# Kernel tuning notes

Measured on AMD Instinct MI355X. Metric: run time of the kernel, lower is better.

Reference implementation:

```python
import jax, jax.numpy as jnp
import numpy as np

BH, S, D = 32, 2048, 128

def setup_inputs() -> dict:
    key = jax.random.key(0)
    k1, k2, k3, k4 = jax.random.split(key, 4)
    q = jax.random.normal(k1, (BH, S, D), dtype=jnp.float32)
    k = jax.random.normal(k2, (BH, S, D), dtype=jnp.float32)
    v = jax.random.normal(k3, (BH, S, D), dtype=jnp.float32)
    scale_factor = jax.random.normal(k4, (S, S), dtype=jnp.float32)
    return {"q": q, "k": k, "v": v, "scale_factor": scale_factor, "dropout_p": 1}

def reference(q, k, v, scale_factor, dropout_p):
    # qk: [BH, Sq, Sk]
    qk = jnp.einsum('bqd,bkd->bqk', q, k)
    scaled_qk = qk * scale_factor  # per-element (non-scalar) scale, broadcast over BH
    p = jax.nn.softmax(scaled_qk, axis=-1)
    # Dropout(p=0.0) is identity; then mul by scalar dropout_p
    p = p * dropout_p
    out = jnp.einsum('bqk,bkd->bqd', p, v)
    return out
```

## Files before the change

### kernel.cpp

```cpp
#include <hip/hip_runtime.h>

#define S_LEN 2048
#define D_DIM 128
#define BQ 128
#define BK 32
#define NITER (S_LEN / BK)
#define NITER2 (NITER / 2)

typedef float f32x4 __attribute__((ext_vector_type(4)));
typedef short s16x8 __attribute__((ext_vector_type(8)));
typedef short s16x4 __attribute__((ext_vector_type(4)));
typedef unsigned int u32;

#if __has_builtin(__builtin_amdgcn_exp2f)
#define EXP2(x) __builtin_amdgcn_exp2f(x)
#else
#define EXP2(x) exp2f(x)
#endif

__device__ __forceinline__ u32 pack_trunc(float x0, float x1) {
    return __builtin_amdgcn_perm(__float_as_uint(x1), __float_as_uint(x0), 0x07060302u);
}
__device__ __forceinline__ u32 pack_rne(float x0, float x1) {
    return __builtin_amdgcn_perm(__float_as_uint(x1) + 0x8000u,
                                 __float_as_uint(x0) + 0x8000u, 0x07060302u);
}

#define GLOAD16(g, l) \
    __builtin_amdgcn_global_load_lds((const __attribute__((address_space(1))) u32*)(g), \
                                     (__attribute__((address_space(3))) u32*)(l), 16, 0, 0)

#if __has_builtin(__builtin_amdgcn_mfma_f32_16x16x16bf16_1k)
__device__ __forceinline__ f32x4 MFMA16(s16x4 a, s16x4 b, f32x4 c) {
    return __builtin_amdgcn_mfma_f32_16x16x16bf16_1k(a, b, c, 0, 0, 0);
}
#else
__device__ __forceinline__ f32x4 MFMA16(s16x4 a, s16x4 b, f32x4 c) {
    asm("v_mfma_f32_16x16x16_bf16 %0, %1, %2, %0" : "+v"(c) : "v"(a), "v"(b));
    return c;
}
#endif

#if __has_builtin(__builtin_amdgcn_permlane16_swap) && __has_builtin(__builtin_amdgcn_permlane32_swap)
#define BFLY(x, OP)                                                                       \
    {                                                                                     \
        auto p_ = __builtin_amdgcn_permlane16_swap(__float_as_uint(x), __float_as_uint(x), false, false); \
        x = OP(__uint_as_float(p_[0]), __uint_as_float(p_[1]));                           \
        auto q_ = __builtin_amdgcn_permlane32_swap(__float_as_uint(x), __float_as_uint(x), false, false); \
        x = OP(__uint_as_float(q_[0]), __uint_as_float(q_[1]));                           \
    }
#else
#define BFLY(x, OP)                      \
    {                                    \
        x = OP(x, __shfl_xor(x, 16));    \
        x = OP(x, __shfl_xor(x, 32));    \
    }
#endif
__device__ __forceinline__ float fadd_(float a, float b) { return a + b; }

__global__ void prep_k(const float* __restrict__ K, unsigned short* __restrict__ Kc) {
    const int t  = blockIdx.x * 256 + threadIdx.x;
    const int c  = t & 15;
    const int s  = (t >> 4) & (S_LEN - 1);
    const int bh = t >> 15;
    const float* src = K + ((size_t)bh * S_LEN + s) * D_DIM + c * 8;
    const float4 a = *(const float4*)src;
    const float4 b = *(const float4*)(src + 4);
    const float x[8] = {a.x,a.y,a.z,a.w,b.x,b.y,b.z,b.w};
    u32 h[4], l[4];
    #pragma unroll
    for (int i = 0; i < 4; ++i) {
        const float x0 = x[2*i], x1 = x[2*i+1];
        h[i] = pack_trunc(x0, x1);
        const float r0 = x0 - __uint_as_float(__float_as_uint(x0) & 0xFFFF0000u);
        const float r1 = x1 - __uint_as_float(__float_as_uint(x1) & 0xFFFF0000u);
        l[i] = pack_trunc(r0, r1);
    }
    const int kt = s >> 5, r = s & 31, rl = r & 7;
    unsigned short* base = Kc + ((((size_t)bh * NITER + kt) * 32 + r) << 8);
    *(uint4*)(base + (((2*c)     ^ rl) << 3)) = make_uint4(h[0],h[1],h[2],h[3]);
    *(uint4*)(base + (((2*c + 1) ^ rl) << 3)) = make_uint4(l[0],l[1],l[2],l[3]);
}

__global__ void prep_v(const float* __restrict__ V, unsigned short* __restrict__ Vt) {
    const int t  = blockIdx.x * 256 + threadIdx.x;
    const int d  = t & 127;
    const int kt = (t >> 7) & (NITER - 1);
    const int bh = t >> 13;
    const float* src = V + (((size_t)bh * NITER + kt) * BK) * D_DIM + d;
    const int dt = d >> 4, lr = d & 15;
    unsigned short* base = Vt + ((((size_t)bh * NITER + kt) * 8 + dt) << 9);
    #pragma unroll
    for (int q = 0; q < 4; ++q) {
        u32 w0 = pack_rne(src[(q*4+0) * D_DIM],    src[(q*4+1) * D_DIM]);
        u32 w1 = pack_rne(src[(q*4+2) * D_DIM],    src[(q*4+3) * D_DIM]);
        u32 w2 = pack_rne(src[(16+q*4+0) * D_DIM], src[(16+q*4+1) * D_DIM]);
        u32 w3 = pack_rne(src[(16+q*4+2) * D_DIM], src[(16+q*4+3) * D_DIM]);
        *(uint4*)(base + ((q * 16 + lr) << 3)) = make_uint4(w0, w1, w2, w3);
    }
}

__global__ __launch_bounds__(512, 2)
void attn_fused(const float* __restrict__ Q, const unsigned short* __restrict__ Kc,
                const unsigned short* __restrict__ Vt, const float* __restrict__ SF,
                const int* __restrict__ DP, float* __restrict__ OUT)
{
    __shared__ __align__(16) unsigned short sK[2][2][32 * 256];
    __shared__ float mlx[4][2][16][2];

    const int bh   = blockIdx.y;
    const int q0   = blockIdx.x * BQ;
    const int tid  = threadIdx.x;
    const int w    = tid >> 6;
    const int par  = w >> 2;
    const int wq   = w & 3;
    const int lane = tid & 63;
    const int quad = lane >> 4;
    const int lr   = lane & 15;
    const int rl   = lr & 7;

    const size_t bh_off = (size_t)bh * S_LEN * D_DIM;
    const float LOG2E = 1.4426950408889634f;

    s16x8 qhi[2][4], qlo[2][4];
    int qrow[2];
    #pragma unroll
    for (int g = 0; g < 2; ++g) {
        qrow[g] = q0 + wq * 32 + g * 16 + lr;
        const float* qr = Q + bh_off + (size_t)qrow[g] * D_DIM + quad * 8;
        #pragma unroll
        for (int d0 = 0; d0 < 4; ++d0) {
            const float4 u0 = *(const float4*)(qr + d0 * 32);
            const float4 u1 = *(const float4*)(qr + d0 * 32 + 4);
            const float x[8] = {u0.x,u0.y,u0.z,u0.w,u1.x,u1.y,u1.z,u1.w};
            union { u32 w4[4]; s16x8 v; } H, L;
            #pragma unroll
            for (int i = 0; i < 4; ++i) {
                const float x0 = x[2*i], x1 = x[2*i+1];
                H.w4[i] = pack_trunc(x0, x1);
                const float r0 = x0 - __uint_as_float(__float_as_uint(x0) & 0xFFFF0000u);
                const float r1 = x1 - __uint_as_float(__float_as_uint(x1) & 0xFFFF0000u);
                L.w4[i] = pack_trunc(r0, r1);
            }
            qhi[g][d0] = H.v; qlo[g][d0] = L.v;
        }
    }

    f32x4 Oacc[2][8] = {};
    float mrow[2] = {-INFINITY, -INFINITY};
    float lrow[2] = {0.f, 0.f};

    const unsigned short* KtBase = Kc + (((size_t)bh * NITER) << 13);
    const unsigned short* VtBase = Vt + (((size_t)bh * NITER) << 12) + (lane << 3);

    {
        const unsigned short* K0 = KtBase + ((size_t)par << 13);
        #pragma unroll
        for (int i = 0; i < 4; ++i)
            GLOAD16(K0 + (wq * 4 + i) * 512 + lane * 8, &sK[0][par][(wq * 4 + i) * 512]);
    }

    const float* sfq[2];
    f32x4 sf0[2], sf1[2];
    {
        const f32x4 l2e = {LOG2E, LOG2E, LOG2E, LOG2E};
        #pragma unroll
        for (int g = 0; g < 2; ++g) {
            sfq[g] = SF + (size_t)qrow[g] * S_LEN + quad * 4;
            sf0[g] = *(const f32x4*)(sfq[g] + par * 32) * l2e;
            sf1[g] = *(const f32x4*)(sfq[g] + par * 32 + 16) * l2e;
        }
    }

    for (int it = 0; it < NITER2; ++it) {
        const int p = it & 1;
        __syncthreads();

        uint4 vreg[8];
        {
            const unsigned short* Vk = VtBase + ((size_t)(2 * it + par) << 12);
            #pragma unroll
            for (int dt = 0; dt < 8; ++dt)
                vreg[dt] = *(const uint4*)(Vk + (dt << 9));
        }

        f32x4 nf0[2], nf1[2];
        const bool more = (it + 1 < NITER2);
        if (more) {
            const unsigned short* Kn = KtBase + ((size_t)(2 * it + 2 + par) << 13);
            #pragma unroll
            for (int i = 0; i < 4; ++i)
                GLOAD16(Kn + (wq * 4 + i) * 512 + lane * 8, &sK[1 - p][par][(wq * 4 + i) * 512]);
            const f32x4 l2e = {LOG2E, LOG2E, LOG2E, LOG2E};
            #pragma unroll
            for (int g = 0; g < 2; ++g) {
                nf0[g] = *(const f32x4*)(sfq[g] + (2 * it + 2 + par) * 32) * l2e;
                nf1[g] = *(const f32x4*)(sfq[g] + (2 * it + 2 + par) * 32 + 16) * l2e;
            }
        }

        const unsigned short* sKp = sK[p][par];
        f32x4 acc[2][2] = {};
        __builtin_amdgcn_s_setprio(1);
        #pragma unroll
        for (int nt = 0; nt < 2; ++nt) {
            const unsigned short* rowp = sKp + (nt * 16 + lr) * 256;
            #pragma unroll
            for (int d0 = 0; d0 < 4; ++d0) {
                const int uh = (8 * d0 + 2 * quad) ^ rl;
                const s16x8 kh8 = *(const s16x8*)(rowp + (uh << 3));
                const s16x8 kl8 = *(const s16x8*)(rowp + ((uh ^ 1) << 3));
                #pragma unroll
                for (int g = 0; g < 2; ++g) {
                    acc[g][nt] = __builtin_amdgcn_mfma_f32_16x16x32_bf16(kh8, qlo[g][d0], acc[g][nt], 0, 0, 0);
                    acc[g][nt] = __builtin_amdgcn_mfma_f32_16x16x32_bf16(kl8, qhi[g][d0], acc[g][nt], 0, 0, 0);
                    acc[g][nt] = __builtin_amdgcn_mfma_f32_16x16x32_bf16(kh8, qhi[g][d0], acc[g][nt], 0, 0, 0);
                }
            }
        }
        __builtin_amdgcn_s_setprio(0);

        union PB { u32 w2[2]; s16x4 v; } B0[2], B1[2];
        #pragma unroll
        for (int g = 0; g < 2; ++g) {
            const f32x4 t0 = acc[g][0] * sf0[g];
            const f32x4 t1 = acc[g][1] * sf1[g];
            float mx = fmaxf(fmaxf(fmaxf(t0[0], t0[1]), fmaxf(t0[2], t0[3])),
                             fmaxf(fmaxf(t1[0], t1[1]), fmaxf(t1[2], t1[3])));
            BFLY(mx, fmaxf);
            const float mnew = fmaxf(mrow[g], mx);
            if (!__all(mnew == mrow[g])) {
                const float al = EXP2(mrow[g] - mnew);
                mrow[g] = mnew;
                lrow[g] *= al;
                const f32x4 alv = {al, al, al, al};
                #pragma unroll
                for (int dt = 0; dt < 8; ++dt)
                    Oacc[g][dt] *= alv;
            }
            const float m = mrow[g];
            f32x4 P0, P1;
            #pragma unroll
            for (int r = 0; r < 4; ++r) {
                P0[r] = EXP2(t0[r] - m);
                P1[r] = EXP2(t1[r] - m);
            }
            float rs = ((P0[0] + P0[1]) + (P0[2] + P0[3])) + ((P1[0] + P1[1]) + (P1[2] + P1[3]));
            BFLY(rs, fadd_);
            lrow[g] += rs;
            B0[g].w2[0] = pack_rne(P0[0], P0[1]); B0[g].w2[1] = pack_rne(P0[2], P0[3]);
            B1[g].w2[0] = pack_rne(P1[0], P1[1]); B1[g].w2[1] = pack_rne(P1[2], P1[3]);
        }

        __builtin_amdgcn_s_setprio(1);
        #pragma unroll
        for (int dt = 0; dt < 8; ++dt) {
            union { uint4 u; struct { s16x4 a0; s16x4 a1; } s; } vv;
            vv.u = vreg[dt];
            #pragma unroll
            for (int g = 0; g < 2; ++g) {
                Oacc[g][dt] = MFMA16(vv.s.a0, B0[g].v, Oacc[g][dt]);
                Oacc[g][dt] = MFMA16(vv.s.a1, B1[g].v, Oacc[g][dt]);
            }
        }
        __builtin_amdgcn_s_setprio(0);

        if (more) {
            #pragma unroll
            for (int g = 0; g < 2; ++g) { sf0[g] = nf0[g]; sf1[g] = nf1[g]; }
        }
    }

    __syncthreads();
    float* obuf = (float*)&sK[0][0][0];
    if (par) {
        #pragma unroll
        for (int g = 0; g < 2; ++g) {
            mlx[wq][g][lr][0] = mrow[g];
            mlx[wq][g][lr][1] = lrow[g];
            #pragma unroll
            for (int dt = 0; dt < 8; ++dt)
                *(f32x4*)(obuf + ((((wq * 2 + g) * 8 + dt) * 64 + lane) << 2)) = Oacc[g][dt];
        }
    }
    __syncthreads();
    if (!par) {
        const float dpf = (float)DP[0];
        #pragma unroll
        for (int g = 0; g < 2; ++g) {
            const float m_o = mlx[wq][g][lr][0];
            const float l_o = mlx[wq][g][lr][1];
            const float ms  = fmaxf(mrow[g], m_o);
            const float se  = EXP2(mrow[g] - ms);
            const float so  = EXP2(m_o - ms);
            const float ls  = se * lrow[g] + so * l_o;
            const float fe  = se * dpf / ls;
            const float fo  = so * dpf / ls;
            const f32x4 fev = {fe, fe, fe, fe};
            const f32x4 fov = {fo, fo, fo, fo};
            float* orow = OUT + bh_off + (size_t)qrow[g] * D_DIM + quad * 4;
            #pragma unroll
            for (int dt = 0; dt < 8; ++dt) {
                const f32x4 oo = *(const f32x4*)(obuf + ((((wq * 2 + g) * 8 + dt) * 64 + lane) << 2));
                const f32x4 o = Oacc[g][dt] * fev + oo * fov;
                *(f32x4*)(orow + dt * 16) = o;
            }
        }
    }
}

extern "C" void kernel_launch(void* const* d_in, const int* in_sizes, int n_in,
                              void* d_out, int out_size, void* d_ws, size_t ws_size,
                              hipStream_t stream) {
    const float* q  = (const float*)d_in[0];
    const float* k  = (const float*)d_in[1];
    const float* v  = (const float*)d_in[2];
    const float* sf = (const float*)d_in[3];
    const int*   dp = (const int*)d_in[4];
    float* out = (float*)d_out;

    const size_t kc_ushorts = (size_t)32 * NITER * 32 * 256;
    unsigned short* Kc = (unsigned short*)d_ws;
    unsigned short* Vt = Kc + kc_ushorts;

    prep_k<<<4096, 256, 0, stream>>>(k, Kc);
    prep_v<<<1024, 256, 0, stream>>>(v, Vt);
    dim3 grid(S_LEN / BQ, 32);
    attn_fused<<<grid, dim3(512), 0, stream>>>(q, Kc, Vt, sf, dp, out);
}
```

Before: 382.8 us.

## Halve query tile and split KV tiles into 16-key halves per wave pair

The query block shrinks from 128 to 64 rows with 256-thread blocks instead of 512. The two wave groups now split each 32-key K/V tile into two 16-key halves rather than taking alternate whole tiles. This halves shared memory and per-wave accumulator and V-register use, which should allow more resident blocks and smaller, more numerous blocks for load balance. The cost is more blocks and smaller MFMA work per sync, and each loop iteration now does half the work, so barrier and softmax overhead per key rises.

```diff
diff --git a/kernel.cpp b/kernel.cpp
--- a/kernel.cpp
+++ b/kernel.cpp
@@ -2,10 +2,10 @@
 
 #define S_LEN 2048
 #define D_DIM 128
-#define BQ 128
+#define BQ 64
 #define BK 32
 #define NITER (S_LEN / BK)
-#define NITER2 (NITER / 2)
+#define HITER 64
 
 typedef float f32x4 __attribute__((ext_vector_type(4)));
 typedef short s16x8 __attribute__((ext_vector_type(8)));
@@ -100,20 +100,20 @@
     }
 }
 
-__global__ __launch_bounds__(512, 2)
+__global__ __launch_bounds__(256, 4)
 void attn_fused(const float* __restrict__ Q, const unsigned short* __restrict__ Kc,
                 const unsigned short* __restrict__ Vt, const float* __restrict__ SF,
                 const int* __restrict__ DP, float* __restrict__ OUT)
 {
-    __shared__ __align__(16) unsigned short sK[2][2][32 * 256];
-    __shared__ float mlx[4][2][16][2];
+    __shared__ __align__(16) unsigned short sK[2][2][16 * 256];
+    __shared__ float mlx[2][2][16][2];
 
     const int bh   = blockIdx.y;
     const int q0   = blockIdx.x * BQ;
     const int tid  = threadIdx.x;
     const int w    = tid >> 6;
-    const int par  = w >> 2;
-    const int wq   = w & 3;
+    const int par  = w >> 1;
+    const int wq   = w & 1;
     const int lane = tid & 63;
     const int quad = lane >> 4;
     const int lr   = lane & 15;
@@ -151,82 +151,74 @@
     float lrow[2] = {0.f, 0.f};
 
     const unsigned short* KtBase = Kc + (((size_t)bh * NITER) << 13);
-    const unsigned short* VtBase = Vt + (((size_t)bh * NITER) << 12) + (lane << 3);
+    const unsigned short* VtBase = Vt + (((size_t)bh * NITER) << 12) + (lane << 3) + (par << 2);
 
     {
-        const unsigned short* K0 = KtBase + ((size_t)par << 13);
+        const unsigned short* K0 = KtBase + ((size_t)par << 12);
         #pragma unroll
         for (int i = 0; i < 4; ++i)
             GLOAD16(K0 + (wq * 4 + i) * 512 + lane * 8, &sK[0][par][(wq * 4 + i) * 512]);
     }
 
     const float* sfq[2];
-    f32x4 sf0[2], sf1[2];
+    f32x4 sf[2];
     {
         const f32x4 l2e = {LOG2E, LOG2E, LOG2E, LOG2E};
         #pragma unroll
         for (int g = 0; g < 2; ++g) {
             sfq[g] = SF + (size_t)qrow[g] * S_LEN + quad * 4;
-            sf0[g] = *(const f32x4*)(sfq[g] + par * 32) * l2e;
-            sf1[g] = *(const f32x4*)(sfq[g] + par * 32 + 16) * l2e;
-        }
-    }
-
-    for (int it = 0; it < NITER2; ++it) {
+            sf[g] = *(const f32x4*)(sfq[g] + par * 16) * l2e;
+        }
+    }
+
+    for (int it = 0; it < HITER; ++it) {
         const int p = it & 1;
         __syncthreads();
 
-        uint4 vreg[8];
+        uint2 vreg[8];
         {
-            const unsigned short* Vk = VtBase + ((size_t)(2 * it + par) << 12);
+            const unsigned short* Vk = VtBase + ((size_t)it << 12);
             #pragma unroll
             for (int dt = 0; dt < 8; ++dt)
-                vreg[dt] = *(const uint4*)(Vk + (dt << 9));
-        }
-
-        f32x4 nf0[2], nf1[2];
-        const bool more = (it + 1 < NITER2);
+                vreg[dt] = *(const uint2*)(Vk + (dt << 9));
+        }
+
+        f32x4 nf[2];
+        const bool more = (it + 1 < HITER);
         if (more) {
-            const unsigned short* Kn = KtBase + ((size_t)(2 * it + 2 + par) << 13);
+            const int tn = 2 * (it + 1) + par;
+            const unsigned short* Kn = KtBase + ((size_t)tn << 12);
             #pragma unroll
             for (int i = 0; i < 4; ++i)
                 GLOAD16(Kn + (wq * 4 + i) * 512 + lane * 8, &sK[1 - p][par][(wq * 4 + i) * 512]);
             const f32x4 l2e = {LOG2E, LOG2E, LOG2E, LOG2E};
             #pragma unroll
+            for (int g = 0; g < 2; ++g)
+                nf[g] = *(const f32x4*)(sfq[g] + tn * 16) * l2e;
+        }
+
+        const unsigned short* rowp = sK[p][par] + lr * 256;
+        f32x4 acc[2] = {};
+        __builtin_amdgcn_s_setprio(1);
+        #pragma unroll
+        for (int d0 = 0; d0 < 4; ++d0) {
+            const int uh = (8 * d0 + 2 * quad) ^ rl;
+            const s16x8 kh8 = *(const s16x8*)(rowp + (uh << 3));
+            const s16x8 kl8 = *(const s16x8*)(rowp + ((uh ^ 1) << 3));
+            #pragma unroll
             for (int g = 0; g < 2; ++g) {
-                nf0[g] = *(const f32x4*)(sfq[g] + (2 * it + 2 + par) * 32) * l2e;
-                nf1[g] = *(const f32x4*)(sfq[g] + (2 * it + 2 + par) * 32 + 16) * l2e;
-            }
-        }
-
-        const unsigned short* sKp = sK[p][par];
-        f32x4 acc[2][2] = {};
-        __builtin_amdgcn_s_setprio(1);
-        #pragma unroll
-        for (int nt = 0; nt < 2; ++nt) {
-            const unsigned short* rowp = sKp + (nt * 16 + lr) * 256;
-            #pragma unroll
-            for (int d0 = 0; d0 < 4; ++d0) {
-                const int uh = (8 * d0 + 2 * quad) ^ rl;
-                const s16x8 kh8 = *(const s16x8*)(rowp + (uh << 3));
-                const s16x8 kl8 = *(const s16x8*)(rowp + ((uh ^ 1) << 3));
-                #pragma unroll
-                for (int g = 0; g < 2; ++g) {
-                    acc[g][nt] = __builtin_amdgcn_mfma_f32_16x16x32_bf16(kh8, qlo[g][d0], acc[g][nt], 0, 0, 0);
-                    acc[g][nt] = __builtin_amdgcn_mfma_f32_16x16x32_bf16(kl8, qhi[g][d0], acc[g][nt], 0, 0, 0);
-                    acc[g][nt] = __builtin_amdgcn_mfma_f32_16x16x32_bf16(kh8, qhi[g][d0], acc[g][nt], 0, 0, 0);
-                }
+                acc[g] = __builtin_amdgcn_mfma_f32_16x16x32_bf16(kh8, qlo[g][d0], acc[g], 0, 0, 0);
+                acc[g] = __builtin_amdgcn_mfma_f32_16x16x32_bf16(kl8, qhi[g][d0], acc[g], 0, 0, 0);
+                acc[g] = __builtin_amdgcn_mfma_f32_16x16x32_bf16(kh8, qhi[g][d0], acc[g], 0, 0, 0);
             }
         }
         __builtin_amdgcn_s_setprio(0);
 
-        union PB { u32 w2[2]; s16x4 v; } B0[2], B1[2];
+        union PB { u32 w2[2]; s16x4 v; } B[2];
         #pragma unroll
         for (int g = 0; g < 2; ++g) {
-            const f32x4 t0 = acc[g][0] * sf0[g];
-            const f32x4 t1 = acc[g][1] * sf1[g];
-            float mx = fmaxf(fmaxf(fmaxf(t0[0], t0[1]), fmaxf(t0[2], t0[3])),
-                             fmaxf(fmaxf(t1[0], t1[1]), fmaxf(t1[2], t1[3])));
+            const f32x4 t0 = acc[g] * sf[g];
+            float mx = fmaxf(fmaxf(t0[0], t0[1]), fmaxf(t0[2], t0[3]));
             BFLY(mx, fmaxf);
             const float mnew = fmaxf(mrow[g], mx);
             if (!__all(mnew == mrow[g])) {
@@ -239,35 +231,30 @@
                     Oacc[g][dt] *= alv;
             }
             const float m = mrow[g];
-            f32x4 P0, P1;
-            #pragma unroll
-            for (int r = 0; r < 4; ++r) {
+            f32x4 P0;
+            #pragma unroll
+            for (int r = 0; r < 4; ++r)
                 P0[r] = EXP2(t0[r] - m);
-                P1[r] = EXP2(t1[r] - m);
-            }
-            float rs = ((P0[0] + P0[1]) + (P0[2] + P0[3])) + ((P1[0] + P1[1]) + (P1[2] + P1[3]));
+            float rs = (P0[0] + P0[1]) + (P0[2] + P0[3]);
             BFLY(rs, fadd_);
             lrow[g] += rs;
-            B0[g].w2[0] = pack_rne(P0[0], P0[1]); B0[g].w2[1] = pack_rne(P0[2], P0[3]);
-            B1[g].w2[0] = pack_rne(P1[0], P1[1]); B1[g].w2[1] = pack_rne(P1[2], P1[3]);
+            B[g].w2[0] = pack_rne(P0[0], P0[1]); B[g].w2[1] = pack_rne(P0[2], P0[3]);
         }
 
         __builtin_amdgcn_s_setprio(1);
         #pragma unroll
         for (int dt = 0; dt < 8; ++dt) {
-            union { uint4 u; struct { s16x4 a0; s16x4 a1; } s; } vv;
+            union { uint2 u; s16x4 v; } vv;
             vv.u = vreg[dt];
             #pragma unroll
-            for (int g = 0; g < 2; ++g) {
-                Oacc[g][dt] = MFMA16(vv.s.a0, B0[g].v, Oacc[g][dt]);
-                Oacc[g][dt] = MFMA16(vv.s.a1, B1[g].v, Oacc[g][dt]);
-            }
+            for (int g = 0; g < 2; ++g)
+                Oacc[g][dt] = MFMA16(vv.v, B[g].v, Oacc[g][dt]);
         }
         __builtin_amdgcn_s_setprio(0);
 
         if (more) {
             #pragma unroll
-            for (int g = 0; g < 2; ++g) { sf0[g] = nf0[g]; sf1[g] = nf1[g]; }
+            for (int g = 0; g < 2; ++g) sf[g] = nf[g];
         }
     }
 
@@ -276,8 +263,10 @@
     if (par) {
         #pragma unroll
         for (int g = 0; g < 2; ++g) {
-            mlx[wq][g][lr][0] = mrow[g];
-            mlx[wq][g][lr][1] = lrow[g];
+            if (quad == 0) {
+                mlx[wq][g][lr][0] = mrow[g];
+                mlx[wq][g][lr][1] = lrow[g];
+            }
             #pragma unroll
             for (int dt = 0; dt < 8; ++dt)
                 *(f32x4*)(obuf + ((((wq * 2 + g) * 8 + dt) * 64 + lane) << 2)) = Oacc[g][dt];
@@ -326,5 +315,5 @@
     prep_k<<<4096, 256, 0, stream>>>(k, Kc);
     prep_v<<<1024, 256, 0, stream>>>(v, Vt);
     dim3 grid(S_LEN / BQ, 32);
-    attn_fused<<<grid, dim3(512), 0, stream>>>(q, Kc, Vt, sf, dp, out);
-}
+    attn_fused<<<grid, dim3(256), 0, stream>>>(q, Kc, Vt, sf, dp, out);
+}
```

Result: slower. 975.0 us (+154.7%).
